# Performance work log

Measured on AMD Instinct MI355X. Metric: run time of the kernel, lower is better.

Reference implementation:

```python
import jax, jax.numpy as jnp
import numpy as np

B, N, W, R = 32, 1024, 128, 4
EPS = 1e-8  # torch CosineSimilarity eps


def _cosine(key, mem):
    # key: (B,K,W), mem: (B,N,W) -> (B,K,N); torch-style eps clamp on norm product
    dot = jnp.einsum('bkw,bnw->bkn', key, mem)
    kn = jnp.linalg.norm(key, axis=-1)[..., None]          # (B,K,1)
    mn = jnp.linalg.norm(mem, axis=-1)[:, None, :]          # (B,1,N)
    return dot / jnp.maximum(kn * mn, EPS)


def setup_inputs() -> dict:
    key = jax.random.key(0)
    ks = jax.random.split(key, 16)
    inp = {
        'memory': jax.random.normal(ks[0], (B, N, W), jnp.float32) * 0.1,
        'temporal_link': jax.random.uniform(ks[1], (B, N, N), jnp.float32) / N,
        'usage': jax.random.uniform(ks[2], (B, 1, N), jnp.float32),
        'precedence': jax.random.uniform(ks[3], (B, 1, N), jnp.float32) / N,
        'read_weights': jax.nn.softmax(jax.random.normal(ks[4], (B, R, N), jnp.float32), axis=-1),
        'read_keys': jax.random.normal(ks[5], (B, R, W), jnp.float32),
        'read_strength': 1.0 + jax.random.uniform(ks[6], (B, R, 1), jnp.float32),
        'read_modes': jax.nn.softmax(jax.random.normal(ks[7], (B, R, 3), jnp.float32), axis=-1),
        'write_key': jax.random.normal(ks[8], (B, W), jnp.float32),
        'write_strength': 1.0 + jax.random.uniform(ks[9], (B, 1), jnp.float32),
        'allocation_gate': jax.random.uniform(ks[10], (B, 1, 1), jnp.float32),
        'write_gate': jax.random.uniform(ks[11], (B, 1, 1), jnp.float32),
        'write_vector': jax.random.normal(ks[12], (B, 1, W), jnp.float32),
        'erase_vector': jax.random.uniform(ks[13], (B, 1, W), jnp.float32),
        'free_gates': jax.random.uniform(ks[14], (B, R, 1), jnp.float32),
    }
    return inp


def reference(memory, temporal_link, usage, precedence, read_weights,
              read_keys, read_strength, read_modes, write_key, write_strength,
              allocation_gate, write_gate, write_vector, erase_vector, free_gates):
    # --- read weights: temporal (fwd/bwd) + content modes ---
    # NOTE: source softmaxes the raw cosine, THEN multiplies by strength
    content_r = jax.nn.softmax(_cosine(read_keys, memory), axis=-1) * read_strength  # (B,R,N)
    fw = jnp.einsum('brn,bmn->brm', read_weights, temporal_link)   # rw @ L^T
    bw = jnp.einsum('brn,bnm->brm', read_weights, temporal_link)   # rw @ L
    new_rw = (fw * read_modes[:, :, 0:1] + bw * read_modes[:, :, 1:2]
              + content_r * read_modes[:, :, 2:3])                 # (B,R,N)
    read_result = jnp.einsum('brn,bnw->brw', new_rw, memory)       # (B,R,W)

    # --- allocation: exclusive cumprod of (unsorted) usage, as in source ---
    cp = jnp.cumprod(usage, axis=-1)
    excl = jnp.concatenate([jnp.ones_like(cp[..., :1]), cp[..., :-1]], axis=-1)
    allocation = (1.0 - usage) * excl                              # (B,1,N)

    # --- write weights (source multiplies strength BEFORE softmax here) ---
    wc = jax.nn.softmax(_cosine(write_key[:, None, :], memory)
                        * write_strength[:, :, None], axis=-1)     # (B,1,N)
    ww = (allocation_gate * (allocation - wc) + wc) * write_gate   # (B,1,N)
    wwT = jnp.swapaxes(ww, 1, 2)                                   # (B,N,1)

    # --- memory erase/write (outer products via broadcasting) ---
    memory_new = memory * (1.0 - wwT * erase_vector) + wwT * write_vector

    # --- temporal link update ---
    grid = wwT + ww                                                # (B,N,N)
    link_new = (1.0 - grid) * temporal_link + wwT * precedence     # (B,N,N)

    # NOTE: source uses a GLOBAL scalar sum of write weights here
    precedence_new = (1.0 - jnp.sum(ww)) * precedence + ww

    # --- usage update (source uses the freshly updated read weights) ---
    retention = jnp.prod(1.0 - free_gates * new_rw, axis=1, keepdims=True)  # (B,1,N)
    usage_new = (usage + ww - usage * ww) * retention

    return (read_result, memory_new, link_new, usage_new, precedence_new, new_rw)
```

## Files before the change

kernel.cpp:

```cpp
#include <hip/hip_runtime.h>
#include <math.h>

#define B 32
#define N 1024
#define W 128
#define R 4
#define EPSC 1e-8f

typedef float f32x4 __attribute__((ext_vector_type(4)));

#define WS_SUM   0
#define WS_KSUM  64
#define WS_BW    256
#define WS_FW    (WS_BW + B*16*R*N)
#define WS_ER    (WS_FW + B*R*N)
#define WS_EW    (WS_ER + B*R*N)
#define WS_WW    (WS_EW + B*N)

#define O_RR    0
#define O_MEM   (O_RR + B*R*W)
#define O_LINK  (O_MEM + B*N*W)
#define O_USAGE (O_LINK + B*N*N)
#define O_PREC  (O_USAGE + B*N)
#define O_NRW   (O_PREC + B*N)

__global__ void k1_scores(const float* __restrict__ mem,
                          const float* __restrict__ rkeys,
                          const float* __restrict__ wkey,
                          const float* __restrict__ wstr,
                          float* __restrict__ ws) {
    int bx = blockIdx.x;
    int b = bx >> 6;
    int n0 = (bx & 63) << 4;
    int t = threadIdx.x;
    __shared__ float keys[5][W];
    __shared__ float knorm[5];
    __shared__ float epart[5][16];
    for (int idx = t; idx < 5 * W; idx += 256) {
        int r = idx >> 7, w = idx & 127;
        keys[r][w] = (r < 4) ? rkeys[(b * R + r) * W + w] : wkey[b * W + w];
    }
    __syncthreads();
    if (t < 160) {
        int kidx = t >> 5, l = t & 31;
        float s = 0.f;
        #pragma unroll
        for (int c = 0; c < 4; ++c) { float v = keys[kidx][l * 4 + c]; s += v * v; }
        #pragma unroll
        for (int st = 1; st <= 16; st <<= 1) s += __shfl_xor(s, st);
        if (l == 0) knorm[kidx] = sqrtf(s);
    }
    __syncthreads();
    int l16 = t & 15;
    int rloc = t >> 4;
    int n = n0 + rloc;
    const float* mrow = mem + ((size_t)(b * N + n)) * W + l16 * 8;
    float4 a  = *reinterpret_cast<const float4*>(mrow);
    float4 a2 = *reinterpret_cast<const float4*>(mrow + 4);
    float mm = a.x*a.x + a.y*a.y + a.z*a.z + a.w*a.w
             + a2.x*a2.x + a2.y*a2.y + a2.z*a2.z + a2.w*a2.w;
    float d[5];
    #pragma unroll
    for (int r = 0; r < 5; ++r) {
        float4 k1v = *reinterpret_cast<const float4*>(&keys[r][l16 * 8]);
        float4 k2v = *reinterpret_cast<const float4*>(&keys[r][l16 * 8 + 4]);
        d[r] = a.x*k1v.x + a.y*k1v.y + a.z*k1v.z + a.w*k1v.w
             + a2.x*k2v.x + a2.y*k2v.y + a2.z*k2v.z + a2.w*k2v.w;
    }
    #pragma unroll
    for (int st = 1; st <= 8; st <<= 1) {
        mm += __shfl_xor(mm, st);
        #pragma unroll
        for (int r = 0; r < 5; ++r) d[r] += __shfl_xor(d[r], st);
    }
    if (l16 == 0) {
        float mn = sqrtf(mm);
        float e[5];
        #pragma unroll
        for (int r = 0; r < 4; ++r) {
            float c = d[r] / fmaxf(knorm[r] * mn, EPSC);
            e[r] = expf(c);
            ws[WS_ER + (b * R + r) * N + n] = e[r];
        }
        float cw = d[4] / fmaxf(knorm[4] * mn, EPSC);
        e[4] = expf(cw * wstr[b]);
        ws[WS_EW + b * N + n] = e[4];
        #pragma unroll
        for (int q = 0; q < 5; ++q) epart[q][rloc] = e[q];
    }
    __syncthreads();
    if (t < 80) {
        int q = t >> 4, i = t & 15;
        float v = epart[q][i];
        #pragma unroll
        for (int st = 1; st <= 8; st <<= 1) v += __shfl_xor(v, st);
        if (i == 0) atomicAdd(&ws[WS_KSUM + b * 5 + q], v);
    }
}

__global__ void k3_link(const float* __restrict__ L,
                        const float* __restrict__ rw,
                        const float* __restrict__ prec,
                        const float* __restrict__ usage,
                        const float* __restrict__ agate,
                        const float* __restrict__ wgate,
                        float* __restrict__ ws,
                        float* __restrict__ out) {
    int bx = blockIdx.x;
    int b = bx >> 4;
    int strip = bx & 15;
    int i0 = strip << 6;
    int t = threadIdx.x;
    int lane = t & 63, wv = t >> 6;
    __shared__ float scratch[256][36];
    __shared__ float ww_l[N];
    __shared__ float rw_row[R][64];
    __shared__ float wpart[4];
    __shared__ float red[4];

    int j0 = 4 * t;

    float4 u4 = *reinterpret_cast<const float4*>(usage + b * N + j0);
    float4 e4 = *reinterpret_cast<const float4*>(ws + WS_EW + b * N + j0);
    float ksw = ws[WS_KSUM + b * 5 + 4];
    float p = u4.x * u4.y * u4.z * u4.w;
    float incl = p;
    #pragma unroll
    for (int s = 1; s <= 32; s <<= 1) {
        float up = __shfl_up(incl, s);
        if (lane >= s) incl *= up;
    }
    if (lane == 63) wpart[wv] = incl;
    for (int idx = t; idx < R * 64; idx += 256) {
        int r = idx >> 6, i = idx & 63;
        rw_row[r][i] = rw[(b * R + r) * N + i0 + i];
    }
    __syncthreads();
    float woff = 1.f;
    #pragma unroll
    for (int w = 0; w < 3; ++w) if (w < wv) woff *= wpart[w];
    float eu = __shfl_up(incl, 1);
    float excl = (lane == 0 ? 1.f : eu) * woff;
    float ag = agate[b], wg = wgate[b];
    float invk = 1.f / ksw;
    float e0 = excl, e1 = e0 * u4.x, e2 = e1 * u4.y, e3 = e2 * u4.z;
    float wc0 = e4.x * invk, wc1 = e4.y * invk, wc2 = e4.z * invk, wc3 = e4.w * invk;
    float4 wwj;
    wwj.x = (ag * ((1.f - u4.x) * e0 - wc0) + wc0) * wg;
    wwj.y = (ag * ((1.f - u4.y) * e1 - wc1) + wc1) * wg;
    wwj.z = (ag * ((1.f - u4.z) * e2 - wc2) + wc2) * wg;
    wwj.w = (ag * ((1.f - u4.w) * e3 - wc3) + wc3) * wg;
    *reinterpret_cast<float4*>(&ww_l[j0]) = wwj;
    float lsum = wwj.x + wwj.y + wwj.z + wwj.w;
    #pragma unroll
    for (int s = 1; s <= 32; s <<= 1) lsum += __shfl_xor(lsum, s);
    if (lane == 0) red[wv] = lsum;
    if (strip == 0)
        *reinterpret_cast<float4*>(ws + WS_WW + b * N + j0) = wwj;
    __syncthreads();
    if (t == 0 && strip == 0)
        atomicAdd(&ws[WS_SUM], red[0] + red[1] + red[2] + red[3]);

    float4 pj  = *reinterpret_cast<const float4*>(prec + b * N + j0);
    float4 rwj[R];
    #pragma unroll
    for (int r = 0; r < R; ++r)
        rwj[r] = *reinterpret_cast<const float4*>(rw + (b * R + r) * N + j0);
    float4 bwa[R];
    #pragma unroll
    for (int r = 0; r < R; ++r) bwa[r] = make_float4(0.f, 0.f, 0.f, 0.f);

    const float* Lr = L + ((size_t)(b * N + i0)) * N + j0;
    float* Or = out + O_LINK + ((size_t)(b * N + i0)) * N + j0;

    int g = t >> 3, kk = t & 7;

    for (int batch = 0; batch < 8; ++batch) {
        float4 v[8];
        #pragma unroll
        for (int k = 0; k < 8; ++k)
            v[k] = *reinterpret_cast<const float4*>(Lr + (size_t)(batch * 8 + k) * N);

        float4 fwp[8];
        #pragma unroll
        for (int k = 0; k < 8; ++k) {
            int row = batch * 8 + k;
            float wi = ww_l[i0 + row];
            float c = 1.f - wi;
            f32x4 o;
            o.x = (c - wwj.x) * v[k].x + wi * pj.x;
            o.y = (c - wwj.y) * v[k].y + wi * pj.y;
            o.z = (c - wwj.z) * v[k].z + wi * pj.z;
            o.w = (c - wwj.w) * v[k].w + wi * pj.w;
            __builtin_nontemporal_store(o,
                reinterpret_cast<f32x4*>(Or + (size_t)row * N));
            float4 f;
            f.x = v[k].x*rwj[0].x + v[k].y*rwj[0].y + v[k].z*rwj[0].z + v[k].w*rwj[0].w;
            f.y = v[k].x*rwj[1].x + v[k].y*rwj[1].y + v[k].z*rwj[1].z + v[k].w*rwj[1].w;
            f.z = v[k].x*rwj[2].x + v[k].y*rwj[2].y + v[k].z*rwj[2].z + v[k].w*rwj[2].w;
            f.w = v[k].x*rwj[3].x + v[k].y*rwj[3].y + v[k].z*rwj[3].z + v[k].w*rwj[3].w;
            fwp[k] = f;
            #pragma unroll
            for (int r = 0; r < R; ++r) {
                float q = rw_row[r][row];
                bwa[r].x += q * v[k].x; bwa[r].y += q * v[k].y;
                bwa[r].z += q * v[k].z; bwa[r].w += q * v[k].w;
            }
        }

        #pragma unroll
        for (int k = 0; k < 8; ++k)
            *reinterpret_cast<float4*>(&scratch[t][k * 4]) = fwp[k];
        __syncthreads();
        float s = 0.f;
        #pragma unroll
        for (int m = 0; m < 32; ++m) s += scratch[kk + 8 * m][g];
        s += __shfl_xor(s, 1);
        s += __shfl_xor(s, 2);
        s += __shfl_xor(s, 4);
        if (kk == 0) {
            int rowk = g >> 2, r = g & 3;
            ws[WS_FW + (b * R + r) * N + i0 + batch * 8 + rowk] = s;
        }
        __syncthreads();
    }

    float* bwout = ws + WS_BW + (size_t)(b * 16 + strip) * R * N;
    #pragma unroll
    for (int r = 0; r < R; ++r)
        *reinterpret_cast<float4*>(bwout + r * N + j0) = bwa[r];
}

__global__ void k4_final(const float* __restrict__ mem,
                         const float* __restrict__ usage,
                         const float* __restrict__ prec,
                         const float* __restrict__ rmodes,
                         const float* __restrict__ rstr,
                         const float* __restrict__ fgates,
                         const float* __restrict__ ev,
                         const float* __restrict__ wvec,
                         float* __restrict__ ws,
                         float* __restrict__ out) {
    int bx = blockIdx.x;
    int b = bx >> 4;
    int n0 = (bx & 15) << 6;
    int t = threadIdx.x;
    __shared__ float nrw[R][64];
    __shared__ float wwl[64];
    __shared__ float rrl[2][R][W];

    {
        int r = t >> 6, nl = t & 63, n = n0 + nl;
        float bs = 0.f;
        #pragma unroll
        for (int tile = 0; tile < 16; ++tile)
            bs += ws[WS_BW + ((size_t)(b * 16 + tile) * R + r) * N + n];
        float fwv = ws[WS_FW + (b * R + r) * N + n];
        float cv  = ws[WS_ER + (b * R + r) * N + n] / ws[WS_KSUM + b * 5 + r]
                    * rstr[b * R + r];
        float m0 = rmodes[(b * R + r) * 3 + 0];
        float m1 = rmodes[(b * R + r) * 3 + 1];
        float m2 = rmodes[(b * R + r) * 3 + 2];
        float v = fwv * m0 + bs * m1 + cv * m2;
        out[O_NRW + (b * R + r) * N + n] = v;
        nrw[r][nl] = v;
    }
    __syncthreads();

    if (t < 64) {
        int n = n0 + t;
        float ret = 1.f;
        #pragma unroll
        for (int r = 0; r < R; ++r) ret *= (1.f - fgates[b * R + r] * nrw[r][t]);
        float u = usage[b * N + n];
        float w = ws[WS_WW + b * N + n];
        out[O_USAGE + b * N + n] = (u + w - u * w) * ret;
        float S = ws[WS_SUM];
        out[O_PREC + b * N + n] = (1.f - S) * prec[b * N + n] + w;
        wwl[t] = w;
    }
    __syncthreads();

    int wi = t & 127, half = t >> 7;
    float er = ev[b * W + wi], wvv = wvec[b * W + wi];
    float acc[R] = {0.f, 0.f, 0.f, 0.f};
    for (int k = 0; k < 32; ++k) {
        int nl = half * 32 + k;
        int n = n0 + nl;
        size_t off = ((size_t)(b * N + n)) * W + wi;
        float m = mem[off];
        float wn = wwl[nl];
        out[O_MEM + off] = m * (1.f - wn * er) + wn * wvv;
        #pragma unroll
        for (int r = 0; r < R; ++r) acc[r] += nrw[r][nl] * m;
    }
    #pragma unroll
    for (int r = 0; r < R; ++r) rrl[half][r][wi] = acc[r];
    __syncthreads();
    for (int idx = t; idx < R * W; idx += 256) {
        int r = idx >> 7, w2 = idx & 127;
        atomicAdd(&out[O_RR + (b * R + r) * W + w2], rrl[0][r][w2] + rrl[1][r][w2]);
    }
}

extern "C" void kernel_launch(void* const* d_in, const int* in_sizes, int n_in,
                              void* d_out, int out_size, void* d_ws, size_t ws_size,
                              hipStream_t stream) {
    const float* mem    = (const float*)d_in[0];
    const float* L      = (const float*)d_in[1];
    const float* usage  = (const float*)d_in[2];
    const float* prec   = (const float*)d_in[3];
    const float* rw     = (const float*)d_in[4];
    const float* rkeys  = (const float*)d_in[5];
    const float* rstr   = (const float*)d_in[6];
    const float* rmodes = (const float*)d_in[7];
    const float* wkey   = (const float*)d_in[8];
    const float* wstr   = (const float*)d_in[9];
    const float* ag     = (const float*)d_in[10];
    const float* wg     = (const float*)d_in[11];
    const float* wv     = (const float*)d_in[12];
    const float* ev     = (const float*)d_in[13];
    const float* fg     = (const float*)d_in[14];
    float* out = (float*)d_out;
    float* ws  = (float*)d_ws;

    (void)hipMemsetAsync(ws, 0, 1024, stream);
    (void)hipMemsetAsync(out, 0, (size_t)B * R * W * sizeof(float), stream);

    k1_scores<<<B * 64, 256, 0, stream>>>(mem, rkeys, wkey, wstr, ws);
    k3_link<<<B * 16, 256, 0, stream>>>(L, rw, prec, usage, ag, wg, ws, out);
    k4_final<<<B * 16, 256, 0, stream>>>(mem, usage, prec, rmodes, rstr, fg, ev, wv, ws, out);
}
```

Before: 84.10 us.

## Double-buffer link tile loads and use per-wave forward-read reduction without block barriers

The link-update kernel now keeps two register buffers and issues the next 8-row batch of temporal-link loads before processing the current one, so memory latency overlaps with compute. The forward-read partial sums are reduced inside each wavefront through its own slice of scratch. Each wave writes to a small per-wave shared array that is combined once at the end. This removes the two block-wide barriers per batch. Launch bounds of 256 threads with 2 blocks per CU are added, and the double buffering raises register pressure, which could cause spills.

```diff
diff --git a/kernel.cpp b/kernel.cpp
--- a/kernel.cpp
+++ b/kernel.cpp
@@ -23,6 +23,8 @@
 #define O_USAGE (O_LINK + B*N*N)
 #define O_PREC  (O_USAGE + B*N)
 #define O_NRW   (O_PREC + B*N)
+
+#define DOT4(a, bv) ((a).x*(bv).x + (a).y*(bv).y + (a).z*(bv).z + (a).w*(bv).w)
 
 __global__ void k1_scores(const float* __restrict__ mem,
                           const float* __restrict__ rkeys,
@@ -57,15 +59,13 @@
     const float* mrow = mem + ((size_t)(b * N + n)) * W + l16 * 8;
     float4 a  = *reinterpret_cast<const float4*>(mrow);
     float4 a2 = *reinterpret_cast<const float4*>(mrow + 4);
-    float mm = a.x*a.x + a.y*a.y + a.z*a.z + a.w*a.w
-             + a2.x*a2.x + a2.y*a2.y + a2.z*a2.z + a2.w*a2.w;
+    float mm = DOT4(a, a) + DOT4(a2, a2);
     float d[5];
     #pragma unroll
     for (int r = 0; r < 5; ++r) {
         float4 k1v = *reinterpret_cast<const float4*>(&keys[r][l16 * 8]);
         float4 k2v = *reinterpret_cast<const float4*>(&keys[r][l16 * 8 + 4]);
-        d[r] = a.x*k1v.x + a.y*k1v.y + a.z*k1v.z + a.w*k1v.w
-             + a2.x*k2v.x + a2.y*k2v.y + a2.z*k2v.z + a2.w*k2v.w;
+        d[r] = DOT4(a, k1v) + DOT4(a2, k2v);
     }
     #pragma unroll
     for (int st = 1; st <= 8; st <<= 1) {
@@ -98,7 +98,8 @@
     }
 }
 
-__global__ void k3_link(const float* __restrict__ L,
+__global__ __launch_bounds__(256, 2) void k3_link(
+                        const float* __restrict__ L,
                         const float* __restrict__ rw,
                         const float* __restrict__ prec,
                         const float* __restrict__ usage,
@@ -115,6 +116,7 @@
     __shared__ float scratch[256][36];
     __shared__ float ww_l[N];
     __shared__ float rw_row[R][64];
+    __shared__ float fwpart[4][64][4];
     __shared__ float wpart[4];
     __shared__ float red[4];
 
@@ -157,9 +159,6 @@
     if (lane == 0) red[wv] = lsum;
     if (strip == 0)
         *reinterpret_cast<float4*>(ws + WS_WW + b * N + j0) = wwj;
-    __syncthreads();
-    if (t == 0 && strip == 0)
-        atomicAdd(&ws[WS_SUM], red[0] + red[1] + red[2] + red[3]);
 
     float4 pj  = *reinterpret_cast<const float4*>(prec + b * N + j0);
     float4 rwj[R];
@@ -173,62 +172,81 @@
     const float* Lr = L + ((size_t)(b * N + i0)) * N + j0;
     float* Or = out + O_LINK + ((size_t)(b * N + i0)) * N + j0;
 
-    int g = t >> 3, kk = t & 7;
-
-    for (int batch = 0; batch < 8; ++batch) {
-        float4 v[8];
-        #pragma unroll
-        for (int k = 0; k < 8; ++k)
-            v[k] = *reinterpret_cast<const float4*>(Lr + (size_t)(batch * 8 + k) * N);
-
-        float4 fwp[8];
-        #pragma unroll
-        for (int k = 0; k < 8; ++k) {
-            int row = batch * 8 + k;
-            float wi = ww_l[i0 + row];
-            float c = 1.f - wi;
-            f32x4 o;
-            o.x = (c - wwj.x) * v[k].x + wi * pj.x;
-            o.y = (c - wwj.y) * v[k].y + wi * pj.y;
-            o.z = (c - wwj.z) * v[k].z + wi * pj.z;
-            o.w = (c - wwj.w) * v[k].w + wi * pj.w;
-            __builtin_nontemporal_store(o,
-                reinterpret_cast<f32x4*>(Or + (size_t)row * N));
-            float4 f;
-            f.x = v[k].x*rwj[0].x + v[k].y*rwj[0].y + v[k].z*rwj[0].z + v[k].w*rwj[0].w;
-            f.y = v[k].x*rwj[1].x + v[k].y*rwj[1].y + v[k].z*rwj[1].z + v[k].w*rwj[1].w;
-            f.z = v[k].x*rwj[2].x + v[k].y*rwj[2].y + v[k].z*rwj[2].z + v[k].w*rwj[2].w;
-            f.w = v[k].x*rwj[3].x + v[k].y*rwj[3].y + v[k].z*rwj[3].z + v[k].w*rwj[3].w;
-            fwp[k] = f;
-            #pragma unroll
-            for (int r = 0; r < R; ++r) {
-                float q = rw_row[r][row];
-                bwa[r].x += q * v[k].x; bwa[r].y += q * v[k].y;
-                bwa[r].z += q * v[k].z; bwa[r].w += q * v[k].w;
-            }
-        }
-
-        #pragma unroll
-        for (int k = 0; k < 8; ++k)
-            *reinterpret_cast<float4*>(&scratch[t][k * 4]) = fwp[k];
-        __syncthreads();
-        float s = 0.f;
-        #pragma unroll
-        for (int m = 0; m < 32; ++m) s += scratch[kk + 8 * m][g];
-        s += __shfl_xor(s, 1);
-        s += __shfl_xor(s, 2);
-        s += __shfl_xor(s, 4);
-        if (kk == 0) {
-            int rowk = g >> 2, r = g & 3;
-            ws[WS_FW + (b * R + r) * N + i0 + batch * 8 + rowk] = s;
-        }
-        __syncthreads();
+    int wbase = t & 192;
+    int half32 = (t & 1) << 5;
+    int oidx = (t & 63) >> 1;
+
+    float4 va[8], vb[8];
+#define LOADB(dst, bat)                                                        \
+    {                                                                          \
+        _Pragma("unroll")                                                      \
+        for (int k = 0; k < 8; ++k)                                            \
+            dst[k] = *reinterpret_cast<const float4*>(                         \
+                Lr + (size_t)((bat) * 8 + k) * N);                             \
+    }
+
+    LOADB(va, 0);
+    __syncthreads();
+    if (t == 0 && strip == 0)
+        atomicAdd(&ws[WS_SUM], red[0] + red[1] + red[2] + red[3]);
+
+#define PROCESS(vv, bat)                                                       \
+    {                                                                          \
+        _Pragma("unroll")                                                      \
+        for (int k = 0; k < 8; ++k) {                                          \
+            int row = (bat) * 8 + k;                                           \
+            float wi = ww_l[i0 + row];                                         \
+            float c = 1.f - wi;                                                \
+            f32x4 o;                                                           \
+            o.x = (c - wwj.x) * vv[k].x + wi * pj.x;                           \
+            o.y = (c - wwj.y) * vv[k].y + wi * pj.y;                           \
+            o.z = (c - wwj.z) * vv[k].z + wi * pj.z;                           \
+            o.w = (c - wwj.w) * vv[k].w + wi * pj.w;                           \
+            __builtin_nontemporal_store(o,                                     \
+                reinterpret_cast<f32x4*>(Or + (size_t)row * N));               \
+            float4 f;                                                          \
+            f.x = DOT4(vv[k], rwj[0]); f.y = DOT4(vv[k], rwj[1]);              \
+            f.z = DOT4(vv[k], rwj[2]); f.w = DOT4(vv[k], rwj[3]);              \
+            *reinterpret_cast<float4*>(&scratch[t][k * 4]) = f;                \
+            _Pragma("unroll")                                                  \
+            for (int r = 0; r < R; ++r) {                                      \
+                float q = rw_row[r][row];                                      \
+                bwa[r].x += q * vv[k].x; bwa[r].y += q * vv[k].y;              \
+                bwa[r].z += q * vv[k].z; bwa[r].w += q * vv[k].w;              \
+            }                                                                  \
+        }                                                                      \
+        float s_ = 0.f;                                                        \
+        _Pragma("unroll")                                                      \
+        for (int m = 0; m < 32; ++m)                                           \
+            s_ += scratch[wbase + half32 + m][oidx];                           \
+        s_ += __shfl_xor(s_, 1);                                               \
+        if (!(t & 1)) fwpart[wv][(bat) * 8 + (oidx >> 2)][oidx & 3] = s_;      \
+    }
+
+    LOADB(vb, 1); PROCESS(va, 0);
+    LOADB(va, 2); PROCESS(vb, 1);
+    LOADB(vb, 3); PROCESS(va, 2);
+    LOADB(va, 4); PROCESS(vb, 3);
+    LOADB(vb, 5); PROCESS(va, 4);
+    LOADB(va, 6); PROCESS(vb, 5);
+    LOADB(vb, 7); PROCESS(va, 6);
+    PROCESS(vb, 7);
+
+    __syncthreads();
+
+    {
+        int row = t >> 2, r = t & 3;
+        float s = fwpart[0][row][r] + fwpart[1][row][r]
+                + fwpart[2][row][r] + fwpart[3][row][r];
+        ws[WS_FW + (b * R + r) * N + i0 + row] = s;
     }
 
     float* bwout = ws + WS_BW + (size_t)(b * 16 + strip) * R * N;
     #pragma unroll
     for (int r = 0; r < R; ++r)
         *reinterpret_cast<float4*>(bwout + r * N + j0) = bwa[r];
+#undef LOADB
+#undef PROCESS
 }
 
 __global__ void k4_final(const float* __restrict__ mem,
```

Result: slower. 225.4 us (+168.0%).
